# Performance work log

Hardware: AMD Instinct MI355X
Metric: run time of the kernel (lower is better)

The kernel has to match this reference:

```python
import math
import jax, jax.numpy as jnp
import numpy as np

B, S, D, H, F, L = 32, 512, 512, 8, 2048, 4
DH = D // H
ALPHA = 1.0
LN_EPS = 1e-12


def setup_inputs() -> dict:
    key = jax.random.key(0)
    ks = jax.random.split(key, 24)
    n = jax.random.normal
    inp = {
        "hidden_states": n(ks[0], (B, S, D), dtype=jnp.float32),
        "position_bias": n(ks[1], (1, H, S, S), dtype=jnp.float32) * 0.02,
        "timestamp": jnp.sort(jax.random.randint(ks[2], (B, S), 0, 10_000_000), axis=-1).astype(jnp.int64),
        # per-layer stacked BERT params
        "Wq": n(ks[3], (L, D, D), dtype=jnp.float32) * 0.02,
        "bq": jnp.zeros((L, D), dtype=jnp.float32),
        "Wk": n(ks[4], (L, D, D), dtype=jnp.float32) * 0.02,
        "bk": jnp.zeros((L, D), dtype=jnp.float32),
        "Wv": n(ks[5], (L, D, D), dtype=jnp.float32) * 0.02,
        "bv": jnp.zeros((L, D), dtype=jnp.float32),
        "Wo": n(ks[6], (L, D, D), dtype=jnp.float32) * 0.02,
        "bo": jnp.zeros((L, D), dtype=jnp.float32),
        "ln1_g": jnp.ones((L, D), dtype=jnp.float32),
        "ln1_b": jnp.zeros((L, D), dtype=jnp.float32),
        "Wi": n(ks[7], (L, D, F), dtype=jnp.float32) * 0.02,
        "bi": jnp.zeros((L, F), dtype=jnp.float32),
        "Wf": n(ks[8], (L, F, D), dtype=jnp.float32) * 0.02,
        "bf": jnp.zeros((L, D), dtype=jnp.float32),
        "ln2_g": jnp.ones((L, D), dtype=jnp.float32),
        "ln2_b": jnp.zeros((L, D), dtype=jnp.float32),
    }
    return inp


def _layernorm(x, g, b):
    mu = jnp.mean(x, axis=-1, keepdims=True)
    var = jnp.mean(jnp.square(x - mu), axis=-1, keepdims=True)
    return (x - mu) * jax.lax.rsqrt(var + LN_EPS) * g + b


def _encoder(hidden_states, position_bias, timestamp,
             Wq, bq, Wk, bk, Wv, bv, Wo, bo, ln1_g, ln1_b,
             Wi, bi, Wf, bf, ln2_g, ln2_b):
    b_, s_, d_ = hidden_states.shape
    # lag-time scale (encoder path: raw timestamps, minutes)
    t = timestamp.astype(jnp.float32)
    lag = (t[:, :, None] - t[:, None, :]) / (60.0 * 1000.0)  # [B,S,S]
    scale = (math.sqrt(DH) - ALPHA / (jnp.maximum(lag, 0.0) + 1.0) + ALPHA)[:, None, :, :]  # [B,1,S,S]

    x = hidden_states
    for l in range(L):
        q = (x @ Wq[l] + bq[l]).reshape(b_, s_, H, DH)
        k = (x @ Wk[l] + bk[l]).reshape(b_, s_, H, DH)
        v = (x @ Wv[l] + bv[l]).reshape(b_, s_, H, DH)
        scores = jnp.einsum('bqhd,bkhd->bhqk', q, k) / scale + position_bias
        probs = jax.nn.softmax(scores, axis=-1)
        ctx = jnp.einsum('bhqk,bkhd->bqhd', probs, v).reshape(b_, s_, d_)
        attn = _layernorm(ctx @ Wo[l] + bo[l] + x, ln1_g[l], ln1_b[l])
        h = jax.nn.gelu(attn @ Wi[l] + bi[l], approximate=False)
        x = _layernorm(h @ Wf[l] + bf[l] + attn, ln2_g[l], ln2_b[l])
    return x


def reference(hidden_states, position_bias, timestamp,
              Wq, bq, Wk, bk, Wv, bv, Wo, bo, ln1_g, ln1_b,
              Wi, bi, Wf, bf, ln2_g, ln2_b):
    return _encoder(hidden_states, position_bias, timestamp,
                    Wq, bq, Wk, bk, Wv, bv, Wo, bo, ln1_g, ln1_b,
                    Wi, bi, Wf, bf, ln2_g, ln2_b)
```

## Files before the change

kernel.cpp:

```cpp
#include <hip/hip_runtime.h>
#include <stdint.h>

#define B_ 32
#define S_ 512
#define D_ 512
#define H_ 8
#define F_ 2048
#define L_ 4
#define DH_ 64
#define M_ (B_*S_)

typedef unsigned short u16;
typedef float f32x4 __attribute__((ext_vector_type(4)));
typedef short bf16x8 __attribute__((ext_vector_type(8)));

__device__ __forceinline__ u16 f2b(float f) {
  unsigned u = __float_as_uint(f);
  u += 0x7FFFu + ((u >> 16) & 1u);
  return (u16)(u >> 16);
}
__device__ __forceinline__ float b2f(u16 u) {
  return __uint_as_float((unsigned)u << 16);
}
__device__ __forceinline__ void gld16(const void* g, void* l) {
  __builtin_amdgcn_global_load_lds((__attribute__((address_space(1))) void*)(void*)g,
                                   (__attribute__((address_space(3))) void*)l, 16, 0, 0);
}
__device__ __forceinline__ f32x4 mfma16(bf16x8 a, bf16x8 b, f32x4 c) {
  return __builtin_amdgcn_mfma_f32_16x16x32_bf16(a, b, c, 0, 0, 0);
}
__device__ __forceinline__ float gelu_fast(float x) {
  float z = 0.7978845608028654f * fmaf(0.044715f * x, x * x, x);
  float e = __expf(2.0f * z);
  float t = 1.0f - 2.0f * __builtin_amdgcn_rcpf(e + 1.0f);
  return 0.5f * x * (1.0f + t);
}

#define LOG2E 1.4426950408889634f

__global__ __launch_bounds__(256) void transpose_w(const float* __restrict__ in,
                                                   u16* __restrict__ out, int R, int C) {
  __shared__ float tile[32][33];
  const int l = blockIdx.z;
  in  += (size_t)l * R * C;
  out += (size_t)l * R * C;
  const int c0 = blockIdx.x * 32, r0 = blockIdx.y * 32;
  const int tx = threadIdx.x, ty = threadIdx.y;
#pragma unroll
  for (int k = 0; k < 4; k++)
    tile[ty + 8*k][tx] = in[(size_t)(r0 + ty + 8*k) * C + c0 + tx];
  __syncthreads();
#pragma unroll
  for (int k = 0; k < 4; k++)
    out[(size_t)(c0 + ty + 8*k) * R + r0 + tx] = f2b(tile[tx][ty + 8*k]);
}

__global__ __launch_bounds__(256) void prep_x(const float* __restrict__ h,
                                              u16* __restrict__ xb) {
  int i = blockIdx.x * 256 + threadIdx.x;
  float4 v = ((const float4*)h)[i];
  ushort4 u; u.x = f2b(v.x); u.y = f2b(v.y); u.z = f2b(v.z); u.w = f2b(v.w);
  ((ushort4*)xb)[i] = u;
}

__global__ __launch_bounds__(256) void prep_pb(const float* __restrict__ pb,
                                               u16* __restrict__ out) {
  const int n0 = (blockIdx.x * 256 + threadIdx.x) * 4;
  const int rowbase = (n0 >> 9) << 9;
  const int nb = n0 & 511;
  const int blk = (nb >> 6) << 6;
  const int lr_ = (nb >> 2) & 15;
  const float* src = pb + rowbase + blk + lr_;
  ushort4 o;
  o.x = f2b(src[0]  * LOG2E);
  o.y = f2b(src[16] * LOG2E);
  o.z = f2b(src[32] * LOG2E);
  o.w = f2b(src[48] * LOG2E);
  ((ushort4*)out)[n0 >> 2] = o;
}

__global__ __launch_bounds__(256) void prep_inv(const int* __restrict__ ts,
                                                u16* __restrict__ invb) {
  const int b  = blockIdx.x >> 7;
  const int rg = blockIdx.x & 127;
  const int wid = threadIdx.x >> 6, lane = threadIdx.x & 63;
  const int i = rg * 4 + wid;
  const float ti = (float)ts[b*S_ + i];
  const int nblk = (lane >> 3) * 64;
  const int l8   = (lane & 7) * 8;
  u16 o[8];
#pragma unroll
  for (int e = 0; e < 8; e++) {
    const int no = l8 + e;
    const int j  = nblk + (no & 3) * 16 + ((no >> 2) & 15);
    float lag = fmaxf((ti - (float)ts[b*S_ + j]) * (1.0f/60000.0f), 0.0f);
    float iv  = (lag + 1.0f) * __builtin_amdgcn_rcpf(fmaf(lag, 9.0f, 8.0f)) * LOG2E;
    o[e] = (u16)(int)rintf((iv - 0.16f) * 524288.0f);
  }
  ushort4 w0 = {o[0], o[1], o[2], o[3]}, w1 = {o[4], o[5], o[6], o[7]};
  u16* out = invb + (((size_t)(b*S_ + i)) << 9) + lane*8;
  *(ushort4*)out       = w0;
  *(ushort4*)(out + 4) = w1;
}

__device__ __forceinline__ void gemm_core(
    const u16* __restrict__ A, const u16* __restrict__ BT,
    const int N, const int K,
    const float* __restrict__ bias, u16* __restrict__ outb, const int epi)
{
  __shared__ u16 As[128*64];
  __shared__ u16 Bs[128*64];
  const int tid = threadIdx.x;
  const int wid = tid >> 6, lane = tid & 63;
  const int wm = (wid >> 1) * 64, wn = (wid & 1) * 64;
  const int lr = lane & 15, quad = lane >> 4;
  const int m0 = blockIdx.x * 128, n0 = blockIdx.y * 128;
  const int l7 = lane & 7, l3 = lane >> 3;
  const int cc = (l7 ^ l3) * 8;
  const int f8 = lr & 7;

  f32x4 acc[4][4];
#pragma unroll
  for (int i = 0; i < 4; i++)
#pragma unroll
    for (int j = 0; j < 4; j++) acc[i][j] = (f32x4){0.f, 0.f, 0.f, 0.f};

  const u16* Ag = A  + (size_t)(m0 + wid*16 + l3)*K + cc;
  const u16* Bg = BT + (size_t)(n0 + l3*4 + wid)*K + cc;
  u16* AsW = As + wid*1024;
  u16* BsW = Bs + wid*1024;

  for (int k0 = 0; k0 < K; k0 += 64) {
    gld16(Ag + k0,                 AsW);
    gld16(Ag + (size_t)8*K + k0,   AsW + 512);
    gld16(Ag + (size_t)64*K + k0,  AsW + 4096);
    gld16(Ag + (size_t)72*K + k0,  AsW + 4608);
    gld16(Bg + k0,                 BsW);
    gld16(Bg + (size_t)32*K + k0,  BsW + 512);
    gld16(Bg + (size_t)64*K + k0,  BsW + 4096);
    gld16(Bg + (size_t)96*K + k0,  BsW + 4608);
    __syncthreads();
#pragma unroll
    for (int kh = 0; kh < 2; kh++) {
      bf16x8 af[4], bfr[4];
#pragma unroll
      for (int i = 0; i < 4; i++)
        af[i]  = *(const bf16x8*)(As + (wm + i*16 + lr)*64 + (((kh*4 + quad) ^ f8) * 8));
#pragma unroll
      for (int j = 0; j < 4; j++)
        bfr[j] = *(const bf16x8*)(Bs + (wn + j*16 + lr)*64 + (((kh*4 + quad) ^ f8) * 8));
#pragma unroll
      for (int i = 0; i < 4; i++)
#pragma unroll
        for (int j = 0; j < 4; j++)
          acc[i][j] = mfma16(af[i], bfr[j], acc[i][j]);
    }
    __syncthreads();
  }

  const int nb = n0 + wn + lr*4;
  float4 b4 = *(const float4*)(bias + nb);
  float bn[4] = {b4.x, b4.y, b4.z, b4.w};

  if (epi == 3) {
#pragma unroll
    for (int i = 0; i < 4; i++) {
      const int m = m0 + wm + i*16 + quad*4;
      const int bb_ = m >> 9, sr = m & 511;
#pragma unroll
      for (int j = 0; j < 4; j++) {
        const int n = nb + j;
        const int hh = n >> 6, dd = n & 63;
        ushort4 o;
        o.x = f2b(acc[i][j][0] + bn[j]);
        o.y = f2b(acc[i][j][1] + bn[j]);
        o.z = f2b(acc[i][j][2] + bn[j]);
        o.w = f2b(acc[i][j][3] + bn[j]);
        *(ushort4*)(outb + (((size_t)((bb_*H_ + hh)*DH_ + dd)) << 9) + sr) = o;
      }
    }
  } else if (epi == 2) {
#pragma unroll
    for (int i = 0; i < 4; i++) {
#pragma unroll
      for (int r = 0; r < 4; r++) {
        const size_t m = (size_t)(m0 + wm + i*16 + quad*4 + r);
        ushort4 o;
        o.x = f2b(gelu_fast(acc[i][0][r] + bn[0]));
        o.y = f2b(gelu_fast(acc[i][1][r] + bn[1]));
        o.z = f2b(gelu_fast(acc[i][2][r] + bn[2]));
        o.w = f2b(gelu_fast(acc[i][3][r] + bn[3]));
        *(ushort4*)(outb + m*N + nb) = o;
      }
    }
  } else {
#pragma unroll
    for (int i = 0; i < 4; i++) {
#pragma unroll
      for (int r = 0; r < 4; r++) {
        const size_t m = (size_t)(m0 + wm + i*16 + quad*4 + r);
        ushort4 o;
        o.x = f2b(acc[i][0][r] + bn[0]);
        o.y = f2b(acc[i][1][r] + bn[1]);
        o.z = f2b(acc[i][2][r] + bn[2]);
        o.w = f2b(acc[i][3][r] + bn[3]);
        *(ushort4*)(outb + m*N + nb) = o;
      }
    }
  }
}

__global__ __launch_bounds__(256) void gemm_kernel(
    const u16* A, const u16* BT, int N, int K,
    const float* bias, u16* outb, int epi)
{
  gemm_core(A, BT, N, K, bias, outb, epi);
}

__global__ __launch_bounds__(256) void gemm_qkv_kernel(
    const u16* A, const u16* BTq, size_t zstride, int K,
    const float* b0, const float* b1, const float* b2,
    u16* out0, u16* out1, u16* out2)
{
  const int z = blockIdx.z;
  const u16* BT = BTq + (size_t)z * zstride;
  const float* bias = (z == 0) ? b0 : (z == 1) ? b1 : b2;
  u16* outb = (z == 0) ? out0 : (z == 1) ? out1 : out2;
  gemm_core(A, BT, 512, K, bias, outb, (z == 2) ? 3 : 0);
}

__global__ __launch_bounds__(256) void gemm64_kernel(
    const u16* __restrict__ A, const u16* __restrict__ BT,
    const int N, const int K,
    const float* __restrict__ bias, const u16* __restrict__ resb,
    float* __restrict__ outf)
{
  __shared__ u16 As[64*64];
  __shared__ u16 Bs[128*64];
  const int tid = threadIdx.x;
  const int wid = tid >> 6, lane = tid & 63;
  const int wm = (wid >> 1) * 32, wn = (wid & 1) * 64;
  const int lr = lane & 15, quad = lane >> 4;
  const int m0 = blockIdx.x * 64, n0 = blockIdx.y * 128;
  const int l7 = lane & 7, l3 = lane >> 3;
  const int cc = (l7 ^ l3) * 8;
  const int f8 = lr & 7;

  f32x4 acc[2][4];
#pragma unroll
  for (int i = 0; i < 2; i++)
#pragma unroll
    for (int j = 0; j < 4; j++) acc[i][j] = (f32x4){0.f, 0.f, 0.f, 0.f};

  const u16* Ag = A  + (size_t)(m0 + wid*8 + l3)*K + cc;
  const u16* Bg = BT + (size_t)(n0 + l3*4 + wid)*K + cc;
  u16* AsW = As + wid*512;
  u16* BsW = Bs + wid*1024;

  for (int k0 = 0; k0 < K; k0 += 64) {
    gld16(Ag + k0,                AsW);
    gld16(Ag + (size_t)32*K + k0, AsW + 2048);
    gld16(Bg + k0,                 BsW);
    gld16(Bg + (size_t)32*K + k0,  BsW + 512);
    gld16(Bg + (size_t)64*K + k0,  BsW + 4096);
    gld16(Bg + (size_t)96*K + k0,  BsW + 4608);
    __syncthreads();
#pragma unroll
    for (int kh = 0; kh < 2; kh++) {
      bf16x8 af[2], bfr[4];
#pragma unroll
      for (int i = 0; i < 2; i++)
        af[i]  = *(const bf16x8*)(As + (wm + i*16 + lr)*64 + (((kh*4 + quad) ^ f8) * 8));
#pragma unroll
      for (int j = 0; j < 4; j++)
        bfr[j] = *(const bf16x8*)(Bs + (wn + j*16 + lr)*64 + (((kh*4 + quad) ^ f8) * 8));
#pragma unroll
      for (int i = 0; i < 2; i++)
#pragma unroll
        for (int j = 0; j < 4; j++)
          acc[i][j] = mfma16(af[i], bfr[j], acc[i][j]);
    }
    __syncthreads();
  }

  const int nb = n0 + wn + lr*4;
  float4 b4 = *(const float4*)(bias + nb);
  float bn[4] = {b4.x, b4.y, b4.z, b4.w};

#pragma unroll
  for (int i = 0; i < 2; i++) {
#pragma unroll
    for (int r = 0; r < 4; r++) {
      const size_t m = (size_t)(m0 + wm + i*16 + quad*4 + r);
      ushort4 rq = *(const ushort4*)(resb + m*N + nb);
      float4 ov;
      ov.x = acc[i][0][r] + bn[0] + b2f(rq.x);
      ov.y = acc[i][1][r] + bn[1] + b2f(rq.y);
      ov.z = acc[i][2][r] + bn[2] + b2f(rq.z);
      ov.w = acc[i][3][r] + bn[3] + b2f(rq.w);
      *(float4*)(outf + m*N + nb) = ov;
    }
  }
}

__global__ __launch_bounds__(256) void ln_kernel(
    const float* __restrict__ y, const float* __restrict__ g, const float* __restrict__ bta,
    float* __restrict__ outf, u16* __restrict__ outb)
{
  const int lane = threadIdx.x & 63;
  const int row = blockIdx.x*4 + (threadIdx.x >> 6);
  const float* yr = y + (size_t)row*D_ + lane*8;
  float4 a0 = *(const float4*)yr;
  float4 a1 = *(const float4*)(yr + 4);
  float v[8] = {a0.x, a0.y, a0.z, a0.w, a1.x, a1.y, a1.z, a1.w};
  float s = 0.f;
#pragma unroll
  for (int e = 0; e < 8; e++) s += v[e];
#pragma unroll
  for (int m = 1; m < 64; m <<= 1) s += __shfl_xor(s, m);
  const float mu = s * (1.0f/512.0f);
  float q = 0.f;
#pragma unroll
  for (int e = 0; e < 8; e++) { float d = v[e] - mu; q += d*d; }
#pragma unroll
  for (int m = 1; m < 64; m <<= 1) q += __shfl_xor(q, m);
  const float rs = rsqrtf(q * (1.0f/512.0f) + 1e-12f);
  float4 g0 = *(const float4*)(g + lane*8);
  float4 g1 = *(const float4*)(g + lane*8 + 4);
  float4 b0 = *(const float4*)(bta + lane*8);
  float4 b1 = *(const float4*)(bta + lane*8 + 4);
  float gg[8] = {g0.x, g0.y, g0.z, g0.w, g1.x, g1.y, g1.z, g1.w};
  float bb[8] = {b0.x, b0.y, b0.z, b0.w, b1.x, b1.y, b1.z, b1.w};
  float o[8];
#pragma unroll
  for (int e = 0; e < 8; e++) o[e] = (v[e] - mu) * rs * gg[e] + bb[e];
  if (outf) {
    float4 w0 = {o[0], o[1], o[2], o[3]}, w1 = {o[4], o[5], o[6], o[7]};
    *(float4*)(outf + (size_t)row*D_ + lane*8)     = w0;
    *(float4*)(outf + (size_t)row*D_ + lane*8 + 4) = w1;
  }
  ushort4 u0 = {f2b(o[0]), f2b(o[1]), f2b(o[2]), f2b(o[3])};
  ushort4 u1 = {f2b(o[4]), f2b(o[5]), f2b(o[6]), f2b(o[7])};
  *(ushort4*)(outb + (size_t)row*D_ + lane*8)     = u0;
  *(ushort4*)(outb + (size_t)row*D_ + lane*8 + 4) = u1;
}

__global__ __launch_bounds__(256, 4) void attn_kernel(
    const u16* __restrict__ qb, const u16* __restrict__ kb, const u16* __restrict__ vt,
    const u16* __restrict__ pb16, const u16* __restrict__ invb, u16* __restrict__ cb)
{
  __shared__ u16 QPs[64*64];
  __shared__ u16 Ks[64*64], Vs[64*64], PBs[64*64], INVs[64*64];
  const int b = blockIdx.x, it = blockIdx.y, h = blockIdx.z;
  const int i0 = it * 64;
  const int tid = threadIdx.x, wid = tid >> 6, lane = tid & 63;
  const int lr = lane & 15, quad = lane >> 4;
  const int l7 = lane & 7, l3 = lane >> 3;
  const int cc = (l7 ^ l3) * 8;
  const int f8 = lr & 7;
  const int rr = wid*8 + l3;

  const u16* qg  = qb + ((size_t)(b*S_ + i0))*D_ + h*DH_;
  const u16* kg  = kb + ((size_t)b*S_)*D_ + h*DH_;
  const u16* vg  = vt + ((size_t)(b*H_ + h)*DH_)*S_;
  const u16* pbg = pb16 + ((size_t)(h*S_ + i0))*S_;
  const u16* ivg = invb + ((size_t)(b*S_ + i0))*S_;

  gld16(qg + (size_t)rr*D_ + cc,        QPs + wid*512);
  gld16(qg + (size_t)(rr+32)*D_ + cc,   QPs + 2048 + wid*512);
  __syncthreads();

  bf16x8 aq0 = *(const bf16x8*)(QPs + (wid*16 + lr)*64 + ((quad ^ f8) * 8));
  bf16x8 aq1 = *(const bf16x8*)(QPs + (wid*16 + lr)*64 + (((quad ^ f8) ^ 4) * 8));
  u16* Pw = QPs + wid*1024;

  f32x4 O[4]; float lacc[4];
#pragma unroll
  for (int dt = 0; dt < 4; dt++) O[dt] = (f32x4){0.f, 0.f, 0.f, 0.f};
#pragma unroll
  for (int r = 0; r < 4; r++) lacc[r] = 0.f;
  const int lrh = lr >> 3;

  for (int t8 = 0; t8 < 8; t8++) {
    const int j0 = t8 * 64;
    gld16(kg + (size_t)(j0+rr)*D_ + cc,       Ks   + wid*512);
    gld16(kg + (size_t)(j0+rr+32)*D_ + cc,    Ks   + 2048 + wid*512);
    gld16(vg + (size_t)rr*S_ + j0 + cc,       Vs   + wid*512);
    gld16(vg + (size_t)(rr+32)*S_ + j0 + cc,  Vs   + 2048 + wid*512);
    gld16(pbg + (size_t)rr*S_ + j0 + cc,      PBs  + wid*512);
    gld16(pbg + (size_t)(rr+32)*S_ + j0 + cc, PBs  + 2048 + wid*512);
    gld16(ivg + (size_t)rr*S_ + j0 + cc,      INVs + wid*512);
    gld16(ivg + (size_t)(rr+32)*S_ + j0 + cc, INVs + 2048 + wid*512);
    __syncthreads();

    f32x4 s[4];
#pragma unroll
    for (int jt = 0; jt < 4; jt++) {
      const u16* kr = Ks + (jt*16 + lr)*64;
      bf16x8 bk0 = *(const bf16x8*)(kr + ((quad ^ f8) * 8));
      bf16x8 bk1 = *(const bf16x8*)(kr + (((quad ^ f8) ^ 4) * 8));
      f32x4 z = (f32x4){0.f, 0.f, 0.f, 0.f};
      z = mfma16(aq0, bk0, z);
      z = mfma16(aq1, bk1, z);
      s[jt] = z;
    }
#pragma unroll
    for (int r = 0; r < 4; r++) {
      const int rowl = quad*4 + r;
      const int r7 = rowl & 7;
      const int tbase = (wid*16 + rowl)*64 + ((((lr >> 1) ^ r7) << 3) | ((lr & 1) << 2));
      ushort4 ivq = *(const ushort4*)(INVs + tbase);
      ushort4 pbq = *(const ushort4*)(PBs + tbase);
      const u16 ive[4] = {ivq.x, ivq.y, ivq.z, ivq.w};
      const u16 pbe[4] = {pbq.x, pbq.y, pbq.z, pbq.w};
      const int pbase = rowl*64;
      float pa = 0.f;
#pragma unroll
      for (int jt = 0; jt < 4; jt++) {
        float iv  = fmaf((float)ive[jt], 0x1p-19f, 0.16f);
        float pbf = b2f(pbe[jt]);
        float p = __builtin_amdgcn_exp2f(fmaf(s[jt][r], iv, pbf));
        pa += p;
        const int idx = (((jt*2 + lrh) ^ r7) * 8) + l7;
        Pw[pbase + idx] = f2b(p);
      }
      lacc[r] += pa;
    }
    bf16x8 ap0 = *(const bf16x8*)(Pw + lr*64 + ((quad ^ f8) * 8));
    bf16x8 ap1 = *(const bf16x8*)(Pw + lr*64 + (((quad ^ f8) ^ 4) * 8));
#pragma unroll
    for (int dt = 0; dt < 4; dt++) {
      const u16* vr = Vs + (dt*16 + lr)*64;
      bf16x8 bv0 = *(const bf16x8*)(vr + ((quad ^ f8) * 8));
      bf16x8 bv1 = *(const bf16x8*)(vr + (((quad ^ f8) ^ 4) * 8));
      O[dt] = mfma16(ap0, bv0, O[dt]);
      O[dt] = mfma16(ap1, bv1, O[dt]);
    }
    __syncthreads();
  }

#pragma unroll
  for (int r = 0; r < 4; r++) {
    float sum = lacc[r];
#pragma unroll
    for (int m = 1; m < 16; m <<= 1) sum += __shfl_xor(sum, m);
    const float inv = __builtin_amdgcn_rcpf(sum);
    const size_t row = (size_t)(b*S_ + i0 + wid*16 + quad*4 + r);
#pragma unroll
    for (int dt = 0; dt < 4; dt++)
      cb[row*D_ + h*DH_ + dt*16 + lr] = f2b(O[dt][r] * inv);
  }
}

extern "C" void kernel_launch(void* const* d_in, const int* in_sizes, int n_in,
                              void* d_out, int out_size, void* d_ws, size_t ws_size,
                              hipStream_t stream)
{
  const float* hidden = (const float*)d_in[0];
  const float* pbias  = (const float*)d_in[1];
  const int*   ts     = (const int*)d_in[2];
  const float* Wq = (const float*)d_in[3];   const float* bq  = (const float*)d_in[4];
  const float* Wk = (const float*)d_in[5];   const float* bk  = (const float*)d_in[6];
  const float* Wv = (const float*)d_in[7];   const float* bv  = (const float*)d_in[8];
  const float* Wo = (const float*)d_in[9];   const float* bo  = (const float*)d_in[10];
  const float* l1g = (const float*)d_in[11]; const float* l1b = (const float*)d_in[12];
  const float* Wi = (const float*)d_in[13];  const float* bi  = (const float*)d_in[14];
  const float* Wf = (const float*)d_in[15];  const float* bfw = (const float*)d_in[16];
  const float* l2g = (const float*)d_in[17]; const float* l2b = (const float*)d_in[18];

  char* w = (char*)d_ws;
  u16* xb    = (u16*)w; w += (size_t)M_*D_*2;
  u16* qb    = (u16*)w; w += (size_t)M_*D_*2;
  u16* kbuf  = (u16*)w; w += (size_t)M_*D_*2;
  u16* vtw   = (u16*)w; w += (size_t)M_*D_*2;
  u16* cbuf  = (u16*)w; w += (size_t)M_*D_*2;
  u16* attnb = (u16*)w; w += (size_t)M_*D_*2;
  float* yf  = (float*)w; w += (size_t)M_*D_*4;
  u16* WqkvT = (u16*)w; w += (size_t)3*L_*D_*D_*2;
  u16* WoT   = (u16*)w; w += (size_t)L_*D_*D_*2;
  u16* WiT   = (u16*)w; w += (size_t)L_*D_*F_*2;
  u16* WfT   = (u16*)w; w += (size_t)L_*F_*D_*2;
  u16* pbb   = (u16*)w; w += (size_t)H_*S_*S_*2;
  u16* invb  = (u16*)w; w += (size_t)B_*S_*S_*2;
  u16* hb    = qb;

  float* x = (float*)d_out;

  const size_t WD = (size_t)D_*D_;
  const size_t WF = (size_t)D_*F_;
  dim3 tb(32, 8);

  transpose_w<<<dim3(16,16,L_), tb, 0, stream>>>(Wq, WqkvT,           D_, D_);
  transpose_w<<<dim3(16,16,L_), tb, 0, stream>>>(Wk, WqkvT + L_*WD,   D_, D_);
  transpose_w<<<dim3(16,16,L_), tb, 0, stream>>>(Wv, WqkvT + 2*L_*WD, D_, D_);
  transpose_w<<<dim3(16,16,L_), tb, 0, stream>>>(Wo, WoT,             D_, D_);
  transpose_w<<<dim3(64,16,L_), tb, 0, stream>>>(Wi, WiT,             D_, F_);
  transpose_w<<<dim3(16,64,L_), tb, 0, stream>>>(Wf, WfT,             F_, D_);
  prep_x<<<dim3(8192), dim3(256), 0, stream>>>(hidden, xb);
  prep_pb<<<dim3(H_*S_*S_/1024), dim3(256), 0, stream>>>(pbias, pbb);
  prep_inv<<<dim3(B_*S_/4), dim3(256), 0, stream>>>(ts, invb);

  for (int l = 0; l < L_; l++) {
    gemm_qkv_kernel<<<dim3(128,4,3), dim3(256), 0, stream>>>(
        xb, WqkvT + l*WD, (size_t)L_*WD, D_,
        bq + l*D_, bk + l*D_, bv + l*D_, qb, kbuf, vtw);
    attn_kernel<<<dim3(B_,8,H_), dim3(256), 0, stream>>>(qb, kbuf, vtw, pbb, invb, cbuf);
    gemm64_kernel<<<dim3(256,4), dim3(256), 0, stream>>>(
        cbuf, WoT + l*WD, D_, D_, bo + l*D_, xb, yf);
    ln_kernel<<<dim3(4096), dim3(256), 0, stream>>>(yf, l1g + l*D_, l1b + l*D_,
                                                    (float*)nullptr, attnb);
    gemm_kernel<<<dim3(128,16), dim3(256), 0, stream>>>(
        attnb, WiT + l*WF, F_, D_, bi + l*F_, hb, 2);
    gemm64_kernel<<<dim3(256,4), dim3(256), 0, stream>>>(
        hb, WfT + l*WF, D_, F_, bfw + l*D_, attnb, yf);
    ln_kernel<<<dim3(4096), dim3(256), 0, stream>>>(yf, l2g + l*D_, l2b + l*D_,
                                                    (l == 3) ? x : (float*)nullptr, xb);
  }
}
```

Baseline: 1.084 ms.

## Double-buffer LDS tiles in GEMM kernels to overlap loads with MFMA

Both GEMM cores now use two LDS buffers per operand and issue the async global-to-LDS loads for the next K tile before computing on the current one. This hides global memory latency behind MFMA work and removes one barrier per tile. In exchange, LDS use per block doubles, which can lower occupancy. The loop also assumes K/64 is even.

```diff
diff --git a/kernel.cpp b/kernel.cpp
--- a/kernel.cpp
+++ b/kernel.cpp
@@ -108,8 +108,8 @@
     const int N, const int K,
     const float* __restrict__ bias, u16* __restrict__ outb, const int epi)
 {
-  __shared__ u16 As[128*64];
-  __shared__ u16 Bs[128*64];
+  __shared__ u16 As0[128*64], Bs0[128*64];
+  __shared__ u16 As1[128*64], Bs1[128*64];
   const int tid = threadIdx.x;
   const int wid = tid >> 6, lane = tid & 63;
   const int wm = (wid >> 1) * 64, wn = (wid & 1) * 64;
@@ -127,10 +127,11 @@
 
   const u16* Ag = A  + (size_t)(m0 + wid*16 + l3)*K + cc;
   const u16* Bg = BT + (size_t)(n0 + l3*4 + wid)*K + cc;
-  u16* AsW = As + wid*1024;
-  u16* BsW = Bs + wid*1024;
-
-  for (int k0 = 0; k0 < K; k0 += 64) {
+  const int wo = wid * 1024;
+
+  auto STAGE = [&](int k0, u16* AsB, u16* BsB) {
+    u16* AsW = AsB + wo;
+    u16* BsW = BsB + wo;
     gld16(Ag + k0,                 AsW);
     gld16(Ag + (size_t)8*K + k0,   AsW + 512);
     gld16(Ag + (size_t)64*K + k0,  AsW + 4096);
@@ -139,22 +140,34 @@
     gld16(Bg + (size_t)32*K + k0,  BsW + 512);
     gld16(Bg + (size_t)64*K + k0,  BsW + 4096);
     gld16(Bg + (size_t)96*K + k0,  BsW + 4608);
-    __syncthreads();
+  };
+  auto COMPUTE = [&](const u16* AsB, const u16* BsB) {
 #pragma unroll
     for (int kh = 0; kh < 2; kh++) {
       bf16x8 af[4], bfr[4];
 #pragma unroll
       for (int i = 0; i < 4; i++)
-        af[i]  = *(const bf16x8*)(As + (wm + i*16 + lr)*64 + (((kh*4 + quad) ^ f8) * 8));
+        af[i]  = *(const bf16x8*)(AsB + (wm + i*16 + lr)*64 + (((kh*4 + quad) ^ f8) * 8));
 #pragma unroll
       for (int j = 0; j < 4; j++)
-        bfr[j] = *(const bf16x8*)(Bs + (wn + j*16 + lr)*64 + (((kh*4 + quad) ^ f8) * 8));
+        bfr[j] = *(const bf16x8*)(BsB + (wn + j*16 + lr)*64 + (((kh*4 + quad) ^ f8) * 8));
 #pragma unroll
       for (int i = 0; i < 4; i++)
 #pragma unroll
         for (int j = 0; j < 4; j++)
           acc[i][j] = mfma16(af[i], bfr[j], acc[i][j]);
     }
+  };
+
+  const int NT = K >> 6;
+  STAGE(0, As0, Bs0);
+  __syncthreads();
+  for (int t = 0; t < NT; t += 2) {
+    STAGE((t + 1) << 6, As1, Bs1);
+    COMPUTE(As0, Bs0);
+    __syncthreads();
+    if (t + 2 < NT) STAGE((t + 2) << 6, As0, Bs0);
+    COMPUTE(As1, Bs1);
     __syncthreads();
   }
 
@@ -235,8 +248,8 @@
     const float* __restrict__ bias, const u16* __restrict__ resb,
     float* __restrict__ outf)
 {
-  __shared__ u16 As[64*64];
-  __shared__ u16 Bs[128*64];
+  __shared__ u16 As0[64*64], Bs0[128*64];
+  __shared__ u16 As1[64*64], Bs1[128*64];
   const int tid = threadIdx.x;
   const int wid = tid >> 6, lane = tid & 63;
   const int wm = (wid >> 1) * 32, wn = (wid & 1) * 64;
@@ -254,32 +267,44 @@
 
   const u16* Ag = A  + (size_t)(m0 + wid*8 + l3)*K + cc;
   const u16* Bg = BT + (size_t)(n0 + l3*4 + wid)*K + cc;
-  u16* AsW = As + wid*512;
-  u16* BsW = Bs + wid*1024;
-
-  for (int k0 = 0; k0 < K; k0 += 64) {
+
+  auto STAGE = [&](int k0, u16* AsB, u16* BsB) {
+    u16* AsW = AsB + wid*512;
+    u16* BsW = BsB + wid*1024;
     gld16(Ag + k0,                AsW);
     gld16(Ag + (size_t)32*K + k0, AsW + 2048);
     gld16(Bg + k0,                 BsW);
     gld16(Bg + (size_t)32*K + k0,  BsW + 512);
     gld16(Bg + (size_t)64*K + k0,  BsW + 4096);
     gld16(Bg + (size_t)96*K + k0,  BsW + 4608);
-    __syncthreads();
+  };
+  auto COMPUTE = [&](const u16* AsB, const u16* BsB) {
 #pragma unroll
     for (int kh = 0; kh < 2; kh++) {
       bf16x8 af[2], bfr[4];
 #pragma unroll
       for (int i = 0; i < 2; i++)
-        af[i]  = *(const bf16x8*)(As + (wm + i*16 + lr)*64 + (((kh*4 + quad) ^ f8) * 8));
+        af[i]  = *(const bf16x8*)(AsB + (wm + i*16 + lr)*64 + (((kh*4 + quad) ^ f8) * 8));
 #pragma unroll
       for (int j = 0; j < 4; j++)
-        bfr[j] = *(const bf16x8*)(Bs + (wn + j*16 + lr)*64 + (((kh*4 + quad) ^ f8) * 8));
+        bfr[j] = *(const bf16x8*)(BsB + (wn + j*16 + lr)*64 + (((kh*4 + quad) ^ f8) * 8));
 #pragma unroll
       for (int i = 0; i < 2; i++)
 #pragma unroll
         for (int j = 0; j < 4; j++)
           acc[i][j] = mfma16(af[i], bfr[j], acc[i][j]);
     }
+  };
+
+  const int NT = K >> 6;
+  STAGE(0, As0, Bs0);
+  __syncthreads();
+  for (int t = 0; t < NT; t += 2) {
+    STAGE((t + 1) << 6, As1, Bs1);
+    COMPUTE(As0, Bs0);
+    __syncthreads();
+    if (t + 2 < NT) STAGE((t + 2) << 6, As0, Bs0);
+    COMPUTE(As1, Bs1);
     __syncthreads();
   }
 
```

After: 1.089 ms. No clear change (+0.4%).
